# Performance work log

Measured on AMD Instinct MI355X. Metric: run time of the kernel, lower is better.

Reference implementation:

```python
import jax, jax.numpy as jnp
import numpy as np

N = 8192
IN_C = 256
OUT_C = 64
ALPHA = 0.2  # LeakyReLU negative slope
NEG_INF = -9e15


def setup_inputs() -> dict:
    key = jax.random.key(0)
    k1, k2, k3, k4 = jax.random.split(key, 4)
    x = jax.random.normal(k1, (N, IN_C), dtype=jnp.float32)
    adjacent = jax.random.randint(k2, (N, N), 0, 2, dtype=jnp.int32)
    # xavier_uniform with gain=1.2: limit = gain * sqrt(6/(fan_in+fan_out))
    lim_w = 1.2 * np.sqrt(6.0 / (IN_C + OUT_C))
    w = jax.random.uniform(k3, (IN_C, OUT_C), dtype=jnp.float32, minval=-lim_w, maxval=lim_w)
    lim_a = 1.2 * np.sqrt(6.0 / (2 * OUT_C + 1))
    a = jax.random.uniform(k4, (2 * OUT_C, 1), dtype=jnp.float32, minval=-lim_a, maxval=lim_a)
    return {"x": x, "adjacent": adjacent, "w": w, "a": a}


def reference(x, adjacent, w, a):
    # h: [N, out]
    h = x @ w
    # e_ij = LeakyReLU(a^T [h_i || h_j]) computed without materializing [N,N,2*out]:
    # split a into source/target halves -> rank-1 broadcast sum.
    a_src = a[:OUT_C, 0]   # [out]
    a_dst = a[OUT_C:, 0]   # [out]
    f_src = h @ a_src      # [N]
    f_dst = h @ a_dst      # [N]
    e = f_src[:, None] + f_dst[None, :]            # [N, N]
    e = jnp.where(e > 0, e, ALPHA * e)             # LeakyReLU
    # mask by adjacency, softmax over neighbors (rows)
    e = jnp.where(adjacent > 0, e, NEG_INF)
    attention = jax.nn.softmax(e, axis=-1)         # [N, N]
    h_prime = attention @ h                        # [N, out]
    # concat=True -> ELU activation
    return jax.nn.elu(h_prime)
```

## Files before the change

### kernel.cpp

```cpp
#include <hip/hip_runtime.h>
#include <hip/hip_bf16.h>

#define N 8192
#define IN_C 256
#define OUT_C 64
#define ALPHA 0.2f
#define L2E 1.44269504f

typedef short bf16x8 __attribute__((ext_vector_type(8)));
typedef float f32x4 __attribute__((ext_vector_type(4)));
typedef unsigned long long u64;

#define OFF_H      0u
#define OFF_HT     2097152u
#define OFF_FS     3145728u
#define OFF_FD     3178496u
#define OFF_FDMAX  3211264u
#define OFF_NUM    3211520u

__global__ __launch_bounds__(256) void k_linear(const float* __restrict__ x,
                                                const float* __restrict__ w,
                                                const float* __restrict__ a,
                                                float* __restrict__ h,
                                                float* __restrict__ fs,
                                                float* __restrict__ fd) {
    __shared__ float wl[IN_C * OUT_C];
    int t = threadIdx.x;
    for (int idx = t; idx < IN_C * OUT_C; idx += 256) wl[idx] = w[idx];
    __syncthreads();
    int i = blockIdx.x * 4 + (t >> 6);
    int c = t & 63;
    const float* xr = x + (size_t)i * IN_C;
    float acc = 0.f;
#pragma unroll 8
    for (int k = 0; k < IN_C; ++k) acc = fmaf(xr[k], wl[k * 64 + c], acc);
    h[(size_t)i * 64 + c] = acc;
    float s = acc * a[c];
    float d = acc * a[64 + c];
#pragma unroll
    for (int off = 32; off > 0; off >>= 1) {
        s += __shfl_xor(s, off, 64);
        d += __shfl_xor(d, off, 64);
    }
    if (c == 0) { fs[i] = s; fd[i] = d; }
}

__global__ __launch_bounds__(256) void k_tr(const float* __restrict__ h,
                                            __hip_bfloat16* __restrict__ ht) {
    __shared__ __hip_bfloat16 lds[64 * 65];
    int t = threadIdx.x;
    int i0 = blockIdx.x * 64;
#pragma unroll
    for (int k = 0; k < 16; ++k) {
        int idx = k * 256 + t;
        int il = idx >> 6, c = idx & 63;
        lds[c * 65 + il] = __float2bfloat16(h[(size_t)(i0 + il) * 64 + c]);
    }
    __syncthreads();
#pragma unroll
    for (int k = 0; k < 16; ++k) {
        int idx = k * 256 + t;
        int c = idx >> 6, il = idx & 63;
        ht[(size_t)c * N + i0 + il] = lds[c * 65 + il];
    }
}

__global__ __launch_bounds__(256) void k_fdmax(const float* __restrict__ fd,
                                               float* __restrict__ out) {
    __shared__ float red[256];
    int t = threadIdx.x;
    float m = -3.4e38f;
    for (int j = t; j < N; j += 256) m = fmaxf(m, fd[j]);
    red[t] = m;
    __syncthreads();
    for (int s = 128; s > 0; s >>= 1) {
        if (t < s) red[t] = fmaxf(red[t], red[t + s]);
        __syncthreads();
    }
    if (t == 0) out[0] = red[0];
}

struct HStage {
    float4 fd0, fd1;
    bf16x8 b0, b1, b2, b3;
};

__device__ __forceinline__ void load_h(HStage& s,
        const float* __restrict__ fdst,
        const unsigned short* __restrict__ pb0, const unsigned short* __restrict__ pb1,
        const unsigned short* __restrict__ pb2, const unsigned short* __restrict__ pb3,
        int jb) {
    s.fd0 = *(const float4*)(fdst + jb);
    s.fd1 = *(const float4*)(fdst + jb + 4);
    s.b0  = *(const bf16x8*)(pb0 + jb);
    s.b1  = *(const bf16x8*)(pb1 + jb);
    s.b2  = *(const bf16x8*)(pb2 + jb);
    s.b3  = *(const bf16x8*)(pb3 + jb);
}

__device__ __forceinline__ void compute_h(const HStage& s,
        u64 m0, u64 m1, u64 m2, u64 m3, int k8, int kg2,
        float fs, float mL, const bf16x8& bones,
        f32x4& acc0, f32x4& acc1, f32x4& acc2, f32x4& acc3, f32x4& acc4) {
    float fdv[8] = {s.fd0.x, s.fd0.y, s.fd0.z, s.fd0.w, s.fd1.x, s.fd1.y, s.fd1.z, s.fd1.w};
    u64 msel[4] = {m0, m1, m2, m3};
    bf16x8 af;
#pragma unroll
    for (int e = 0; e < 8; ++e) {
        int sh = k8 * 8 + kg2 + (e >> 2);
        unsigned bit = (unsigned)(msel[e & 3] >> sh) & 1u;
        float ee = fs + fdv[e];
        float l  = fmaxf(ee, ALPHA * ee);
        float a2 = __builtin_fmaf(l, L2E, -mL);
        float wt = __builtin_amdgcn_exp2f(a2);
        wt = bit ? wt : 0.f;
        __hip_bfloat16 hb = __float2bfloat16(wt);
        union { __hip_bfloat16 b; short s16; } u; u.b = hb;
        af[e] = u.s16;
    }
    acc0 = __builtin_amdgcn_mfma_f32_16x16x32_bf16(af, s.b0, acc0, 0, 0, 0);
    acc1 = __builtin_amdgcn_mfma_f32_16x16x32_bf16(af, s.b1, acc1, 0, 0, 0);
    acc2 = __builtin_amdgcn_mfma_f32_16x16x32_bf16(af, s.b2, acc2, 0, 0, 0);
    acc3 = __builtin_amdgcn_mfma_f32_16x16x32_bf16(af, s.b3, acc3, 0, 0, 0);
    acc4 = __builtin_amdgcn_mfma_f32_16x16x32_bf16(af, bones, acc4, 0, 0, 0);
}

__global__ __launch_bounds__(256, 4) void k_main(
    const int* __restrict__ adj,
    const float* __restrict__ fsrc,
    const float* __restrict__ fdst,
    const float* __restrict__ fdmax_p,
    const unsigned short* __restrict__ ht,
    float* __restrict__ nump,
    float* __restrict__ denp_out,
    int jch, int ns, int groups) {
    __shared__ u64 bits[64 * 34];
    int bid = blockIdx.x;
    int rb = bid & 127;
    int kq = bid >> 7;
    int t = threadIdx.x;
    int w = t >> 6;
    int l = t & 63;
    int r  = l & 15;
    int kg = l >> 4;
    int kg2 = kg * 2;
    int ib0 = rb * 64;
    int i  = ib0 + w * 16 + r;
    int j0 = kq * jch;
    int strideU = groups * 4 + 2;

    for (int rr2 = 0; rr2 < 16; ++rr2) {
        int rowL = w * 16 + rr2;
        const int* src = adj + (size_t)(ib0 + rowL) * N + j0;
        for (int g = 0; g < groups; ++g) {
            int4 v = *(const int4*)(src + g * 256 + l * 4);
            u64 b0 = __ballot(v.x > 0);
            u64 b1 = __ballot(v.y > 0);
            u64 b2 = __ballot(v.z > 0);
            u64 b3 = __ballot(v.w > 0);
            if (l == 0) {
                u64* p = &bits[rowL * strideU + g * 4];
                p[0] = b0; p[1] = b1; p[2] = b2; p[3] = b3;
            }
        }
    }
    __syncthreads();

    float fs  = fsrc[i];
    float fdm = *fdmax_p;
    float e0  = fs + fdm;
    float m   = fmaxf(e0, ALPHA * e0);
    float mL  = m * L2E;

    const unsigned short* pb0 = ht + (size_t)(r)      * N;
    const unsigned short* pb1 = ht + (size_t)(16 + r) * N;
    const unsigned short* pb2 = ht + (size_t)(32 + r) * N;
    const unsigned short* pb3 = ht + (size_t)(48 + r) * N;

    bf16x8 bones;
#pragma unroll
    for (int e = 0; e < 8; ++e) bones[e] = (short)0x3F80;

    f32x4 acc0 = {0.f,0.f,0.f,0.f}, acc1 = {0.f,0.f,0.f,0.f};
    f32x4 acc2 = {0.f,0.f,0.f,0.f}, acc3 = {0.f,0.f,0.f,0.f};
    f32x4 acc4 = {0.f,0.f,0.f,0.f};

    int base = j0 + kg * 8;
    int rowL = w * 16 + r;
    HStage A, B;
    load_h(A, fdst, pb0, pb1, pb2, pb3, base);
    load_h(B, fdst, pb0, pb1, pb2, pb3, base + 32);

#pragma unroll 1
    for (int g = 0; g < groups; ++g) {
        const u64* mp = &bits[rowL * strideU + g * 4];
        u64 m0 = mp[0], m1 = mp[1], m2 = mp[2], m3 = mp[3];
#pragma unroll
        for (int k8 = 0; k8 < 8; ++k8) {
            int ks = g * 8 + k8;
            int nxt = ks + 2 < ns ? ks + 2 : 0;
            if (k8 & 1) {
                compute_h(B, m0, m1, m2, m3, k8, kg2, fs, mL, bones,
                          acc0, acc1, acc2, acc3, acc4);
                load_h(B, fdst, pb0, pb1, pb2, pb3, base + nxt * 32);
            } else {
                compute_h(A, m0, m1, m2, m3, k8, kg2, fs, mL, bones,
                          acc0, acc1, acc2, acc3, acc4);
                load_h(A, fdst, pb0, pb1, pb2, pb3, base + nxt * 32);
            }
        }
    }

    int orow = ib0 + w * 16 + kg * 4;
    float* np = nump + (size_t)kq * N * 64;
#pragma unroll
    for (int rr = 0; rr < 4; ++rr) {
        np[(size_t)(orow + rr) * 64 + 0 * 16 + r] = acc0[rr];
        np[(size_t)(orow + rr) * 64 + 1 * 16 + r] = acc1[rr];
        np[(size_t)(orow + rr) * 64 + 2 * 16 + r] = acc2[rr];
        np[(size_t)(orow + rr) * 64 + 3 * 16 + r] = acc3[rr];
    }
    if (r == 0) {
#pragma unroll
        for (int rr = 0; rr < 4; ++rr) denp_out[kq * N + orow + rr] = acc4[rr];
    }
}

__global__ __launch_bounds__(256) void k_final(const float* __restrict__ nump,
                                               const float* __restrict__ denp,
                                               float* __restrict__ out,
                                               int kqn) {
    int gid = blockIdx.x * 256 + threadIdx.x;
    int base = gid * 4;
    int i = base >> 6;
    float4 num = {0.f, 0.f, 0.f, 0.f};
    float den = 0.f;
    for (int q = 0; q < kqn; ++q) {
        float4 v = *(const float4*)(nump + (size_t)q * (N * 64) + base);
        num.x += v.x; num.y += v.y; num.z += v.z; num.w += v.w;
        den += denp[q * N + i];
    }
    float rd = 1.f / den;
    float4 o;
    o.x = num.x * rd; o.y = num.y * rd; o.z = num.z * rd; o.w = num.w * rd;
    o.x = o.x > 0.f ? o.x : __expf(o.x) - 1.f;
    o.y = o.y > 0.f ? o.y : __expf(o.y) - 1.f;
    o.z = o.z > 0.f ? o.z : __expf(o.z) - 1.f;
    o.w = o.w > 0.f ? o.w : __expf(o.w) - 1.f;
    *(float4*)(out + base) = o;
}

extern "C" void kernel_launch(void* const* d_in, const int* in_sizes, int n_in,
                              void* d_out, int out_size, void* d_ws, size_t ws_size,
                              hipStream_t stream) {
    const float* x   = (const float*)d_in[0];
    const int*   adj = (const int*)d_in[1];
    const float* w   = (const float*)d_in[2];
    const float* a   = (const float*)d_in[3];
    float* out = (float*)d_out;
    char*  ws  = (char*)d_ws;

    float*          h    = (float*)(ws + OFF_H);
    __hip_bfloat16* ht   = (__hip_bfloat16*)(ws + OFF_HT);
    float*          fs   = (float*)(ws + OFF_FS);
    float*          fd   = (float*)(ws + OFF_FD);
    float*          fdm  = (float*)(ws + OFF_FDMAX);
    float*          nump = (float*)(ws + OFF_NUM);

    size_t need8 = (size_t)OFF_NUM + 8ull * N * 64 * 4 + 8ull * N * 4;
    int KQ = (ws_size >= need8) ? 8 : 4;
    float* denp = nump + (size_t)KQ * N * 64;
    int jch = N / KQ;
    int ns  = jch / 32;
    int groups = jch / 256;

    k_linear<<<2048, 256, 0, stream>>>(x, w, a, h, fs, fd);
    k_tr<<<128, 256, 0, stream>>>(h, ht);
    k_fdmax<<<1, 256, 0, stream>>>(fd, fdm);
    k_main<<<KQ * 128, 256, 0, stream>>>(adj, fs, fd, fdm,
                                         (const unsigned short*)ht, nump, denp,
                                         jch, ns, groups);
    k_final<<<512, 256, 0, stream>>>(nump, denp, out, KQ);
}
```

Baseline: 528.1 us.

## Split adjacency bit-packing into separate kernel and pre-swizzle h into MFMA fragments

The adjacency-to-bitmask ballot packing moves out of the main MFMA kernel into a standalone streaming kernel that writes a global bitmask. The main kernel then only copies the small bitmask into LDS. The transposed bf16 h buffer is replaced by a fragment-ordered layout, so each lane does contiguous 16-byte loads at fixed offsets instead of strided rows. This is meant to let the 256MB adjacency read run at full bandwidth, decoupled from the compute kernel's occupancy. The cost is an extra launch and an 8MB bitmask round trip through memory.

```diff
diff --git a/kernel.cpp b/kernel.cpp
--- a/kernel.cpp
+++ b/kernel.cpp
@@ -16,7 +16,8 @@
 #define OFF_FS     3145728u
 #define OFF_FD     3178496u
 #define OFF_FDMAX  3211264u
-#define OFF_NUM    3211520u
+#define OFF_BITS   3211520u
+#define OFF_NUM    11600128u
 
 __global__ __launch_bounds__(256) void k_linear(const float* __restrict__ x,
                                                 const float* __restrict__ w,
@@ -45,23 +46,34 @@
     if (c == 0) { fs[i] = s; fd[i] = d; }
 }
 
-__global__ __launch_bounds__(256) void k_tr(const float* __restrict__ h,
-                                            __hip_bfloat16* __restrict__ ht) {
-    __shared__ __hip_bfloat16 lds[64 * 65];
+__global__ __launch_bounds__(256) void k_frag(const float* __restrict__ h,
+                                              unsigned short* __restrict__ htf) {
+    __shared__ float lds[64 * 65];
     int t = threadIdx.x;
     int i0 = blockIdx.x * 64;
 #pragma unroll
     for (int k = 0; k < 16; ++k) {
         int idx = k * 256 + t;
         int il = idx >> 6, c = idx & 63;
-        lds[c * 65 + il] = __float2bfloat16(h[(size_t)(i0 + il) * 64 + c]);
+        lds[c * 65 + il] = h[(size_t)(i0 + il) * 64 + c];
     }
     __syncthreads();
-#pragma unroll
-    for (int k = 0; k < 16; ++k) {
-        int idx = k * 256 + t;
-        int c = idx >> 6, il = idx & 63;
-        ht[(size_t)c * N + i0 + il] = lds[c * 65 + il];
+    int l = t & 63;
+    int ct = t >> 6;
+    int r = l & 15, kg = l >> 4;
+    int ch = ct * 16 + r;
+#pragma unroll
+    for (int ksl = 0; ksl < 2; ++ksl) {
+        int ks = blockIdx.x * 2 + ksl;
+        int n0 = ksl * 32 + kg * 8;
+        bf16x8 v;
+#pragma unroll
+        for (int e = 0; e < 8; ++e) {
+            __hip_bfloat16 hb = __float2bfloat16(lds[ch * 65 + n0 + e]);
+            union { __hip_bfloat16 b; short s16; } u; u.b = hb;
+            v[e] = u.s16;
+        }
+        *(bf16x8*)(htf + ((size_t)(ks * 4 + ct) * 64 + l) * 8) = v;
     }
 }
 
@@ -80,22 +92,45 @@
     if (t == 0) out[0] = red[0];
 }
 
+__global__ __launch_bounds__(256) void k_pack(const int* __restrict__ adj,
+                                              u64* __restrict__ bits) {
+    const int NW = 2048 * 4;
+    int t = threadIdx.x;
+    int l = t & 63;
+    int wv = (blockIdx.x * 256 + t) >> 6;
+#pragma unroll 1
+    for (int c = wv; c < (N / 256) * N / 1; c += 2 * NW) {
+        int4 v0 = *(const int4*)(adj + (size_t)c * 256 + l * 4);
+        int4 v1 = *(const int4*)(adj + (size_t)(c + NW) * 256 + l * 4);
+        u64 a0 = __ballot(v0.x > 0), a1 = __ballot(v0.y > 0);
+        u64 a2 = __ballot(v0.z > 0), a3 = __ballot(v0.w > 0);
+        u64 b0 = __ballot(v1.x > 0), b1 = __ballot(v1.y > 0);
+        u64 b2 = __ballot(v1.z > 0), b3 = __ballot(v1.w > 0);
+        if (l == 0) {
+            u64* q0 = bits + (size_t)c * 4;
+            q0[0] = a0; q0[1] = a1; q0[2] = a2; q0[3] = a3;
+            u64* q1 = bits + (size_t)(c + NW) * 4;
+            q1[0] = b0; q1[1] = b1; q1[2] = b2; q1[3] = b3;
+        }
+    }
+}
+
 struct HStage {
     float4 fd0, fd1;
     bf16x8 b0, b1, b2, b3;
 };
 
-__device__ __forceinline__ void load_h(HStage& s,
+__device__ __forceinline__ void load_h2(HStage& s,
         const float* __restrict__ fdst,
-        const unsigned short* __restrict__ pb0, const unsigned short* __restrict__ pb1,
-        const unsigned short* __restrict__ pb2, const unsigned short* __restrict__ pb3,
-        int jb) {
+        const unsigned short* __restrict__ hb,
+        int jb, int ksg) {
     s.fd0 = *(const float4*)(fdst + jb);
     s.fd1 = *(const float4*)(fdst + jb + 4);
-    s.b0  = *(const bf16x8*)(pb0 + jb);
-    s.b1  = *(const bf16x8*)(pb1 + jb);
-    s.b2  = *(const bf16x8*)(pb2 + jb);
-    s.b3  = *(const bf16x8*)(pb3 + jb);
+    const unsigned short* p = hb + (size_t)ksg * 2048;
+    s.b0 = *(const bf16x8*)(p);
+    s.b1 = *(const bf16x8*)(p + 512);
+    s.b2 = *(const bf16x8*)(p + 1024);
+    s.b3 = *(const bf16x8*)(p + 1536);
 }
 
 __device__ __forceinline__ void compute_h(const HStage& s,
@@ -125,44 +160,30 @@
     acc4 = __builtin_amdgcn_mfma_f32_16x16x32_bf16(af, bones, acc4, 0, 0, 0);
 }
 
-__global__ __launch_bounds__(256, 4) void k_main(
-    const int* __restrict__ adj,
+__global__ __launch_bounds__(256, 4) void k_mfma(
+    const u64* __restrict__ bitsg,
     const float* __restrict__ fsrc,
     const float* __restrict__ fdst,
     const float* __restrict__ fdmax_p,
-    const unsigned short* __restrict__ ht,
+    const unsigned short* __restrict__ htf,
     float* __restrict__ nump,
     float* __restrict__ denp_out,
     int jch, int ns, int groups) {
     __shared__ u64 bits[64 * 34];
     int bid = blockIdx.x;
-    int rb = bid & 127;
-    int kq = bid >> 7;
-    int t = threadIdx.x;
-    int w = t >> 6;
-    int l = t & 63;
-    int r  = l & 15;
-    int kg = l >> 4;
-    int kg2 = kg * 2;
+    int rb = bid & 127, kq = bid >> 7;
+    int t = threadIdx.x, w = t >> 6, l = t & 63;
+    int r = l & 15, kg = l >> 4, kg2 = kg * 2;
     int ib0 = rb * 64;
-    int i  = ib0 + w * 16 + r;
+    int i = ib0 + w * 16 + r;
     int j0 = kq * jch;
     int strideU = groups * 4 + 2;
-
-    for (int rr2 = 0; rr2 < 16; ++rr2) {
-        int rowL = w * 16 + rr2;
-        const int* src = adj + (size_t)(ib0 + rowL) * N + j0;
-        for (int g = 0; g < groups; ++g) {
-            int4 v = *(const int4*)(src + g * 256 + l * 4);
-            u64 b0 = __ballot(v.x > 0);
-            u64 b1 = __ballot(v.y > 0);
-            u64 b2 = __ballot(v.z > 0);
-            u64 b3 = __ballot(v.w > 0);
-            if (l == 0) {
-                u64* p = &bits[rowL * strideU + g * 4];
-                p[0] = b0; p[1] = b1; p[2] = b2; p[3] = b3;
-            }
-        }
+    int gw = groups * 4;
+    int gbase4 = (j0 >> 8) * 4;
+
+    for (int u = t; u < 64 * gw; u += 256) {
+        int rowL = u / gw, rem = u - rowL * gw;
+        bits[rowL * strideU + rem] = bitsg[(size_t)(ib0 + rowL) * 128 + gbase4 + rem];
     }
     __syncthreads();
 
@@ -172,10 +193,8 @@
     float m   = fmaxf(e0, ALPHA * e0);
     float mL  = m * L2E;
 
-    const unsigned short* pb0 = ht + (size_t)(r)      * N;
-    const unsigned short* pb1 = ht + (size_t)(16 + r) * N;
-    const unsigned short* pb2 = ht + (size_t)(32 + r) * N;
-    const unsigned short* pb3 = ht + (size_t)(48 + r) * N;
+    const unsigned short* hb = htf + l * 8;
+    int ks0 = j0 >> 5;
 
     bf16x8 bones;
 #pragma unroll
@@ -185,11 +204,11 @@
     f32x4 acc2 = {0.f,0.f,0.f,0.f}, acc3 = {0.f,0.f,0.f,0.f};
     f32x4 acc4 = {0.f,0.f,0.f,0.f};
 
-    int base = j0 + kg * 8;
+    int baseJ = j0 + kg * 8;
     int rowL = w * 16 + r;
     HStage A, B;
-    load_h(A, fdst, pb0, pb1, pb2, pb3, base);
-    load_h(B, fdst, pb0, pb1, pb2, pb3, base + 32);
+    load_h2(A, fdst, hb, baseJ, ks0);
+    load_h2(B, fdst, hb, baseJ + 32, ks0 + 1);
 
 #pragma unroll 1
     for (int g = 0; g < groups; ++g) {
@@ -202,11 +221,11 @@
             if (k8 & 1) {
                 compute_h(B, m0, m1, m2, m3, k8, kg2, fs, mL, bones,
                           acc0, acc1, acc2, acc3, acc4);
-                load_h(B, fdst, pb0, pb1, pb2, pb3, base + nxt * 32);
+                load_h2(B, fdst, hb, baseJ + nxt * 32, ks0 + nxt);
             } else {
                 compute_h(A, m0, m1, m2, m3, k8, kg2, fs, mL, bones,
                           acc0, acc1, acc2, acc3, acc4);
-                load_h(A, fdst, pb0, pb1, pb2, pb3, base + nxt * 32);
+                load_h2(A, fdst, hb, baseJ + nxt * 32, ks0 + nxt);
             }
         }
     }
@@ -261,10 +280,11 @@
     char*  ws  = (char*)d_ws;
 
     float*          h    = (float*)(ws + OFF_H);
-    __hip_bfloat16* ht   = (__hip_bfloat16*)(ws + OFF_HT);
+    unsigned short* htf  = (unsigned short*)(ws + OFF_HT);
     float*          fs   = (float*)(ws + OFF_FS);
     float*          fd   = (float*)(ws + OFF_FD);
     float*          fdm  = (float*)(ws + OFF_FDMAX);
+    u64*            bits = (u64*)(ws + OFF_BITS);
     float*          nump = (float*)(ws + OFF_NUM);
 
     size_t need8 = (size_t)OFF_NUM + 8ull * N * 64 * 4 + 8ull * N * 4;
@@ -275,10 +295,10 @@
     int groups = jch / 256;
 
     k_linear<<<2048, 256, 0, stream>>>(x, w, a, h, fs, fd);
-    k_tr<<<128, 256, 0, stream>>>(h, ht);
+    k_frag<<<128, 256, 0, stream>>>(h, htf);
     k_fdmax<<<1, 256, 0, stream>>>(fd, fdm);
-    k_main<<<KQ * 128, 256, 0, stream>>>(adj, fs, fd, fdm,
-                                         (const unsigned short*)ht, nump, denp,
+    k_pack<<<2048, 256, 0, stream>>>(adj, bits);
+    k_mfma<<<KQ * 128, 256, 0, stream>>>(bits, fs, fd, fdm, htf, nump, denp,
                                          jch, ns, groups);
     k_final<<<512, 256, 0, stream>>>(nump, denp, out, KQ);
 }
```

Result: faster. 511.8 us (-3.1%).
